# Performance work log

Hardware: AMD Instinct MI355X
Metric: run time of the kernel (lower is better)

The kernel has to match this reference:

```python
import jax, jax.numpy as jnp
import numpy as np

N = 8192
IN_DIM = 512
OUT_DIM = 64
ALPHA = 0.2  # LeakyReLU negative slope
NEG_FILL = -9e15


def setup_inputs() -> dict:
    key = jax.random.key(0)
    k1, k2, k3, k4 = jax.random.split(key, 4)
    features = jax.random.normal(k1, (N, IN_DIM), dtype=jnp.float32)
    adj = jax.random.randint(k2, (N, N), 0, 2, dtype=jnp.int32)
    # xavier_normal with gain 1.414 ~ sqrt(2)
    W = jax.random.normal(k3, (IN_DIM, OUT_DIM), dtype=jnp.float32) * (1.414 * np.sqrt(2.0 / (IN_DIM + OUT_DIM)))
    a = jax.random.normal(k4, (2 * OUT_DIM, 1), dtype=jnp.float32) * (1.414 * np.sqrt(2.0 / (2 * OUT_DIM + 1)))
    return {"features": features, "adj": adj, "W": W, "a": a}


def reference(features, adj, W, a):
    h = features @ W                      # [N, OUT_DIM]
    h1 = h @ a[:OUT_DIM, :]               # [N, 1]
    h2 = h @ a[OUT_DIM:, :]               # [N, 1]
    e = h1 + h2.T                         # [N, N] broadcast add
    e = jnp.where(e > 0, e, ALPHA * e)    # LeakyReLU
    scores = jnp.where(adj > 0, e, NEG_FILL)
    attention = jax.nn.softmax(scores, axis=-1)
    out = attention @ h                   # [N, OUT_DIM]
    out = jax.nn.elu(out)                 # concat=True branch
    return out
```

## Files before the change

kernel.cpp:

```cpp
#include <hip/hip_runtime.h>
#include <hip/hip_bf16.h>

#define N 8192
#define IN_DIM 512
#define OUT_DIM 64
#define ALPHA 0.2f
#define LOG2E 1.44269504f

typedef __hip_bfloat16 bf16;
typedef __attribute__((ext_vector_type(8))) short bf16x8;
typedef __attribute__((ext_vector_type(4))) float f32x4;
typedef __attribute__((ext_vector_type(4))) int   int4v;
typedef __attribute__((ext_vector_type(4))) float float4v;

__device__ __forceinline__ float u2f(unsigned short u) {
    union { unsigned int i; float f; } c; c.i = ((unsigned int)u) << 16; return c.f;
}

__device__ __forceinline__ uint2 splitpack2(float f0, float f1) {
    unsigned u0 = __float_as_uint(f0), u1 = __float_as_uint(f1);
    unsigned h0 = u0 & 0xFFFF0000u, h1 = u1 & 0xFFFF0000u;
    float l0 = f0 - __uint_as_float(h0);
    float l1 = f1 - __uint_as_float(h1);
    uint2 r;
    r.x = (h0 >> 16) | h1;
    r.y = (__float_as_uint(l0) >> 16) | (__float_as_uint(l1) & 0xFFFF0000u);
    return r;
}

__device__ __forceinline__ bf16x8 as_bf16x8(int a, int b, int c, int d) {
    union { int4v i; bf16x8 b; } u;
    u.i = (int4v){a, b, c, d};
    return u.b;
}

__device__ __forceinline__ unsigned fenc(float f) {
    unsigned u = __float_as_uint(f);
    return (u & 0x80000000u) ? ~u : (u | 0x80000000u);
}
__device__ __forceinline__ float fdec(unsigned e) {
    return (e & 0x80000000u) ? __uint_as_float(e & 0x7FFFFFFFu) : __uint_as_float(~e);
}

__global__ void k_sniff(const unsigned short* __restrict__ feat_u16, int* __restrict__ flag) {
    int lane = threadIdx.x;
    float v = u2f(feat_u16[2 * lane]);
    float av = fabsf(v);
    int ok = (v == 0.f) || (av > 1e-8f && av < 1e8f);
    unsigned long long m = __ballot(ok);
    if (lane == 0) *flag = (__popcll(m) >= 48) ? 1 : 0;
}

__global__ __launch_bounds__(256) void k_prep(const void* __restrict__ Wv,
                                              const int* __restrict__ flag,
                                              unsigned short* __restrict__ WT_hi,
                                              unsigned short* __restrict__ WT_lo,
                                              unsigned* __restrict__ h2enc) {
    if (blockIdx.x == 0 && threadIdx.x == 0) *h2enc = fenc(-3e38f);
    int idx = blockIdx.x * 256 + threadIdx.x;
    int k = idx >> 6, c = idx & 63;
    float w = (*flag) ? u2f(((const unsigned short*)Wv)[idx]) : ((const float*)Wv)[idx];
    unsigned u = __float_as_uint(w);
    unsigned hi = u & 0xFFFF0000u;
    float lo = w - __uint_as_float(hi);
    WT_hi[c * IN_DIM + k] = (unsigned short)(hi >> 16);
    WT_lo[c * IN_DIM + k] = (unsigned short)(__float_as_uint(lo) >> 16);
}

__global__ __launch_bounds__(64) void k_h(const void* __restrict__ featv,
                                          const unsigned short* __restrict__ WT_hi,
                                          const unsigned short* __restrict__ WT_lo,
                                          const void* __restrict__ av,
                                          const int* __restrict__ flag,
                                          float* __restrict__ h1,
                                          float* __restrict__ h2,
                                          unsigned short* __restrict__ hT_hi,
                                          unsigned short* __restrict__ hT_lo,
                                          unsigned* __restrict__ h2enc) {
    const int lane = threadIdx.x & 63;
    const int rsub = lane & 15;
    const int g = lane >> 4;
    const int wrow0 = blockIdx.x * 16;
    const int isbf = *flag;

    f32x4 acc0 = {0.f,0.f,0.f,0.f}, acc1 = {0.f,0.f,0.f,0.f};
    f32x4 acc2 = {0.f,0.f,0.f,0.f}, acc3 = {0.f,0.f,0.f,0.f};

    for (int k0 = 0; k0 < IN_DIM; k0 += 32) {
        const int ka = k0 + g * 8;
        bf16x8 Ah, Al;
        if (isbf) {
            Ah = *(const bf16x8*)((const unsigned short*)featv + (size_t)(wrow0 + rsub) * IN_DIM + ka);
            Al = as_bf16x8(0, 0, 0, 0);
        } else {
            const float* fp = (const float*)featv + (size_t)(wrow0 + rsub) * IN_DIM + ka;
            float4v f0 = *(const float4v*)fp;
            float4v f1 = *(const float4v*)(fp + 4);
            uint2 q0 = splitpack2(f0[0], f0[1]);
            uint2 q1 = splitpack2(f0[2], f0[3]);
            uint2 q2 = splitpack2(f1[0], f1[1]);
            uint2 q3 = splitpack2(f1[2], f1[3]);
            Ah = as_bf16x8((int)q0.x, (int)q1.x, (int)q2.x, (int)q3.x);
            Al = as_bf16x8((int)q0.y, (int)q1.y, (int)q2.y, (int)q3.y);
        }
        const unsigned short* wh = WT_hi + (size_t)rsub * IN_DIM + ka;
        const unsigned short* wl = WT_lo + (size_t)rsub * IN_DIM + ka;
        bf16x8 B0h = *(const bf16x8*)(wh);
        bf16x8 B1h = *(const bf16x8*)(wh + 16 * IN_DIM);
        bf16x8 B2h = *(const bf16x8*)(wh + 32 * IN_DIM);
        bf16x8 B3h = *(const bf16x8*)(wh + 48 * IN_DIM);
        bf16x8 B0l = *(const bf16x8*)(wl);
        bf16x8 B1l = *(const bf16x8*)(wl + 16 * IN_DIM);
        bf16x8 B2l = *(const bf16x8*)(wl + 32 * IN_DIM);
        bf16x8 B3l = *(const bf16x8*)(wl + 48 * IN_DIM);

        acc0 = __builtin_amdgcn_mfma_f32_16x16x32_bf16(Ah, B0h, acc0, 0, 0, 0);
        acc1 = __builtin_amdgcn_mfma_f32_16x16x32_bf16(Ah, B1h, acc1, 0, 0, 0);
        acc2 = __builtin_amdgcn_mfma_f32_16x16x32_bf16(Ah, B2h, acc2, 0, 0, 0);
        acc3 = __builtin_amdgcn_mfma_f32_16x16x32_bf16(Ah, B3h, acc3, 0, 0, 0);
        acc0 = __builtin_amdgcn_mfma_f32_16x16x32_bf16(Ah, B0l, acc0, 0, 0, 0);
        acc1 = __builtin_amdgcn_mfma_f32_16x16x32_bf16(Ah, B1l, acc1, 0, 0, 0);
        acc2 = __builtin_amdgcn_mfma_f32_16x16x32_bf16(Ah, B2l, acc2, 0, 0, 0);
        acc3 = __builtin_amdgcn_mfma_f32_16x16x32_bf16(Ah, B3l, acc3, 0, 0, 0);
        acc0 = __builtin_amdgcn_mfma_f32_16x16x32_bf16(Al, B0h, acc0, 0, 0, 0);
        acc1 = __builtin_amdgcn_mfma_f32_16x16x32_bf16(Al, B1h, acc1, 0, 0, 0);
        acc2 = __builtin_amdgcn_mfma_f32_16x16x32_bf16(Al, B2h, acc2, 0, 0, 0);
        acc3 = __builtin_amdgcn_mfma_f32_16x16x32_bf16(Al, B3h, acc3, 0, 0, 0);
    }

    {
        uint2 s01, s23;
        size_t off;
        s01 = splitpack2(acc0[0], acc0[1]); s23 = splitpack2(acc0[2], acc0[3]);
        off = (size_t)(0 * 16 + rsub) * N + wrow0 + g * 4;
        { uint2 ph; ph.x = s01.x; ph.y = s23.x; *(uint2*)(hT_hi + off) = ph; }
        { uint2 pl; pl.x = s01.y; pl.y = s23.y; *(uint2*)(hT_lo + off) = pl; }
        s01 = splitpack2(acc1[0], acc1[1]); s23 = splitpack2(acc1[2], acc1[3]);
        off = (size_t)(1 * 16 + rsub) * N + wrow0 + g * 4;
        { uint2 ph; ph.x = s01.x; ph.y = s23.x; *(uint2*)(hT_hi + off) = ph; }
        { uint2 pl; pl.x = s01.y; pl.y = s23.y; *(uint2*)(hT_lo + off) = pl; }
        s01 = splitpack2(acc2[0], acc2[1]); s23 = splitpack2(acc2[2], acc2[3]);
        off = (size_t)(2 * 16 + rsub) * N + wrow0 + g * 4;
        { uint2 ph; ph.x = s01.x; ph.y = s23.x; *(uint2*)(hT_hi + off) = ph; }
        { uint2 pl; pl.x = s01.y; pl.y = s23.y; *(uint2*)(hT_lo + off) = pl; }
        s01 = splitpack2(acc3[0], acc3[1]); s23 = splitpack2(acc3[2], acc3[3]);
        off = (size_t)(3 * 16 + rsub) * N + wrow0 + g * 4;
        { uint2 ph; ph.x = s01.x; ph.y = s23.x; *(uint2*)(hT_hi + off) = ph; }
        { uint2 pl; pl.x = s01.y; pl.y = s23.y; *(uint2*)(hT_lo + off) = pl; }
    }

    const float* af = (const float*)av;
    const unsigned short* au = (const unsigned short*)av;
    float a10 = isbf ? u2f(au[rsub])      : af[rsub];
    float a11 = isbf ? u2f(au[16 + rsub]) : af[16 + rsub];
    float a12 = isbf ? u2f(au[32 + rsub]) : af[32 + rsub];
    float a13 = isbf ? u2f(au[48 + rsub]) : af[48 + rsub];
    float a20 = isbf ? u2f(au[64 + rsub])  : af[64 + rsub];
    float a21 = isbf ? u2f(au[80 + rsub])  : af[80 + rsub];
    float a22 = isbf ? u2f(au[96 + rsub])  : af[96 + rsub];
    float a23 = isbf ? u2f(au[112 + rsub]) : af[112 + rsub];
    float s1r[4], s2r[4];
#pragma unroll
    for (int r = 0; r < 4; ++r) {
        s1r[r] = acc0[r] * a10 + acc1[r] * a11 + acc2[r] * a12 + acc3[r] * a13;
        s2r[r] = acc0[r] * a20 + acc1[r] * a21 + acc2[r] * a22 + acc3[r] * a23;
    }
#pragma unroll
    for (int off = 8; off; off >>= 1) {
#pragma unroll
        for (int r = 0; r < 4; ++r) {
            s1r[r] += __shfl_xor(s1r[r], off);
            s2r[r] += __shfl_xor(s2r[r], off);
        }
    }
    float wm = fmaxf(fmaxf(s2r[0], s2r[1]), fmaxf(s2r[2], s2r[3])) * LOG2E;
#pragma unroll
    for (int off = 32; off; off >>= 1) wm = fmaxf(wm, __shfl_xor(wm, off));
    if (lane == 0) atomicMax(h2enc, fenc(wm));

    if (rsub < 4) {
        float v1 = rsub == 0 ? s1r[0] : rsub == 1 ? s1r[1] : rsub == 2 ? s1r[2] : s1r[3];
        float v2 = rsub == 0 ? s2r[0] : rsub == 1 ? s2r[1] : rsub == 2 ? s2r[2] : s2r[3];
        h1[wrow0 + g * 4 + rsub] = v1 * LOG2E;
        h2[wrow0 + g * 4 + rsub] = v2 * LOG2E;
    }
}

__global__ __launch_bounds__(256, 2) void k_attn(const int* __restrict__ adj,
                                                 const float* __restrict__ h1,
                                                 const float* __restrict__ h2,
                                                 const unsigned short* __restrict__ hT_hi,
                                                 const unsigned short* __restrict__ hT_lo,
                                                 const unsigned* __restrict__ h2enc,
                                                 float* __restrict__ pacc,
                                                 float* __restrict__ plner,
                                                 int klen) {
    __shared__ float accs[64][66];
    __shared__ float lredL[4][64];

    const int wave = threadIdx.x >> 6;
    const int lane = threadIdx.x & 63;
    const int rsub = lane & 15;
    const int g = lane >> 4;
    const int row0 = blockIdx.x * 64;
    const int kbid = blockIdx.y;

    const float h2m = fdec(*h2enc);
    float h1r[4], c0[4];
#pragma unroll
    for (int mt = 0; mt < 4; ++mt) {
        h1r[mt] = h1[row0 + mt * 16 + rsub];
        float u = h1r[mt] + h2m;
        c0[mt] = -fmaxf(u, ALPHA * u);
    }

    f32x4 acc[4][4];
#pragma unroll
    for (int mt = 0; mt < 4; ++mt)
#pragma unroll
        for (int ct = 0; ct < 4; ++ct) acc[mt][ct] = (f32x4){0.f, 0.f, 0.f, 0.f};
    float lacc[4] = {0.f, 0.f, 0.f, 0.f};

    const unsigned short* bph = hT_hi + (size_t)rsub * N;
    const unsigned short* bpl = hT_lo + (size_t)rsub * N;

    const int kbeg = kbid * klen + wave * (klen >> 2);
    const int kend = kbeg + (klen >> 2);
    for (int k0 = kbeg; k0 < kend; k0 += 32) {
        const int kb = k0 + g * 8;

        const unsigned short* bh = bph + kb;
        const unsigned short* bl = bpl + kb;
        bf16x8 B0h = *(const bf16x8*)(bh);
        bf16x8 B1h = *(const bf16x8*)(bh + 16 * (size_t)N);
        bf16x8 B2h = *(const bf16x8*)(bh + 32 * (size_t)N);
        bf16x8 B3h = *(const bf16x8*)(bh + 48 * (size_t)N);
        bf16x8 B0l = *(const bf16x8*)(bl);
        bf16x8 B1l = *(const bf16x8*)(bl + 16 * (size_t)N);
        bf16x8 B2l = *(const bf16x8*)(bl + 32 * (size_t)N);
        bf16x8 B3l = *(const bf16x8*)(bl + 48 * (size_t)N);

        float4v hA = *(const float4v*)(h2 + kb);
        float4v hB = *(const float4v*)(h2 + kb + 4);

#pragma unroll
        for (int mt = 0; mt < 4; ++mt) {
            const size_t arow = (size_t)(row0 + mt * 16 + rsub) * N + kb;
            int4v aj0 = *(const int4v*)(adj + arow);
            int4v aj1 = *(const int4v*)(adj + arow + 4);

            float w[8];
#pragma unroll
            for (int j = 0; j < 4; ++j) {
                float u = h1r[mt] + hA[j];
                float s = fmaxf(u, ALPHA * u);
                float e = exp2f(s + c0[mt]);
                w[j] = aj0[j] > 0 ? e : 0.f;
            }
#pragma unroll
            for (int j = 0; j < 4; ++j) {
                float u = h1r[mt] + hB[j];
                float s = fmaxf(u, ALPHA * u);
                float e = exp2f(s + c0[mt]);
                w[4 + j] = aj1[j] > 0 ? e : 0.f;
            }
#pragma unroll
            for (int j = 0; j < 8; ++j) lacc[mt] += w[j];

            uint2 p0 = splitpack2(w[0], w[1]);
            uint2 p1 = splitpack2(w[2], w[3]);
            uint2 p2 = splitpack2(w[4], w[5]);
            uint2 p3 = splitpack2(w[6], w[7]);
            bf16x8 Ahi = as_bf16x8((int)p0.x, (int)p1.x, (int)p2.x, (int)p3.x);
            bf16x8 Alo = as_bf16x8((int)p0.y, (int)p1.y, (int)p2.y, (int)p3.y);

            acc[mt][0] = __builtin_amdgcn_mfma_f32_16x16x32_bf16(Ahi, B0h, acc[mt][0], 0, 0, 0);
            acc[mt][1] = __builtin_amdgcn_mfma_f32_16x16x32_bf16(Ahi, B1h, acc[mt][1], 0, 0, 0);
            acc[mt][2] = __builtin_amdgcn_mfma_f32_16x16x32_bf16(Ahi, B2h, acc[mt][2], 0, 0, 0);
            acc[mt][3] = __builtin_amdgcn_mfma_f32_16x16x32_bf16(Ahi, B3h, acc[mt][3], 0, 0, 0);
            acc[mt][0] = __builtin_amdgcn_mfma_f32_16x16x32_bf16(Ahi, B0l, acc[mt][0], 0, 0, 0);
            acc[mt][1] = __builtin_amdgcn_mfma_f32_16x16x32_bf16(Ahi, B1l, acc[mt][1], 0, 0, 0);
            acc[mt][2] = __builtin_amdgcn_mfma_f32_16x16x32_bf16(Ahi, B2l, acc[mt][2], 0, 0, 0);
            acc[mt][3] = __builtin_amdgcn_mfma_f32_16x16x32_bf16(Ahi, B3l, acc[mt][3], 0, 0, 0);
            acc[mt][0] = __builtin_amdgcn_mfma_f32_16x16x32_bf16(Alo, B0h, acc[mt][0], 0, 0, 0);
            acc[mt][1] = __builtin_amdgcn_mfma_f32_16x16x32_bf16(Alo, B1h, acc[mt][1], 0, 0, 0);
            acc[mt][2] = __builtin_amdgcn_mfma_f32_16x16x32_bf16(Alo, B2h, acc[mt][2], 0, 0, 0);
            acc[mt][3] = __builtin_amdgcn_mfma_f32_16x16x32_bf16(Alo, B3h, acc[mt][3], 0, 0, 0);
        }
    }

#pragma unroll
    for (int mt = 0; mt < 4; ++mt) {
        float l = lacc[mt];
        l += __shfl_xor(l, 16);
        l += __shfl_xor(l, 32);
        if (g == 0) lredL[wave][mt * 16 + rsub] = l;
    }

    if (wave == 0) {
#pragma unroll
        for (int mt = 0; mt < 4; ++mt)
#pragma unroll
            for (int ct = 0; ct < 4; ++ct)
#pragma unroll
                for (int r = 0; r < 4; ++r)
                    accs[mt * 16 + g * 4 + r][ct * 16 + rsub] = acc[mt][ct][r];
    }
    __syncthreads();
#pragma unroll
    for (int w2 = 1; w2 < 4; ++w2) {
        if (wave == w2) {
#pragma unroll
            for (int mt = 0; mt < 4; ++mt)
#pragma unroll
                for (int ct = 0; ct < 4; ++ct)
#pragma unroll
                    for (int r = 0; r < 4; ++r)
                        accs[mt * 16 + g * 4 + r][ct * 16 + rsub] += acc[mt][ct][r];
        }
        __syncthreads();
    }

    float* pa = pacc + (size_t)kbid * (N * OUT_DIM);
#pragma unroll
    for (int p = 0; p < 16; ++p) {
        int idx = p * 256 + threadIdx.x;
        int rl = idx >> 6, col = idx & 63;
        pa[(size_t)(row0 + rl) * OUT_DIM + col] = accs[rl][col];
    }
    if (threadIdx.x < 64)
        plner[(size_t)kbid * N + row0 + threadIdx.x] =
            lredL[0][threadIdx.x] + lredL[1][threadIdx.x] + lredL[2][threadIdx.x] + lredL[3][threadIdx.x];
}

__global__ __launch_bounds__(256) void k_out(const float* __restrict__ pacc,
                                             const float* __restrict__ plner,
                                             const int* __restrict__ flag,
                                             void* __restrict__ outv,
                                             int nkb) {
    int idx = blockIdx.x * 256 + threadIdx.x;
    int row = idx >> 6;
    float v = 0.f, l = 0.f;
    for (int kb = 0; kb < nkb; ++kb) {
        v += pacc[(size_t)kb * (N * OUT_DIM) + idx];
        l += plner[(size_t)kb * N + row];
    }
    float o = l > 0.f ? v / l : 0.f;
    o = o > 0.f ? o : exp2f(o * LOG2E) - 1.f;
    if (*flag) ((bf16*)outv)[idx] = __float2bfloat16(o);
    else       ((float*)outv)[idx] = o;
}

extern "C" void kernel_launch(void* const* d_in, const int* in_sizes, int n_in,
                              void* d_out, int out_size, void* d_ws, size_t ws_size,
                              hipStream_t stream) {
    const void* feat = d_in[0];
    const int* adj = (const int*)d_in[1];
    const void* W = d_in[2];
    const void* a = d_in[3];

    char* ws = (char*)d_ws;
    int*      flag  = (int*)(ws);
    unsigned* h2enc = (unsigned*)(ws + 256);
    float* h1       = (float*)(ws + 4096);
    float* h2       = (float*)(ws + 36864);
    unsigned short* hT_hi = (unsigned short*)(ws + 69632);
    unsigned short* hT_lo = (unsigned short*)(ws + 69632 + 1048576);
    unsigned short* WT_hi = (unsigned short*)(ws + 2166784);
    unsigned short* WT_lo = (unsigned short*)(ws + 2166784 + 65536);
    char* dynbase = ws + 2297856;

    size_t cap = ws_size ? ws_size : ((size_t)1 << 30);
    int nkb = 8;
    while (nkb > 1) {
        size_t need = 2297856 + (size_t)nkb * ((size_t)N * OUT_DIM * 4 + (size_t)N * 4);
        if (need <= cap) break;
        nkb >>= 1;
    }
    float* pacc  = (float*)dynbase;
    float* plner = (float*)(dynbase + (size_t)nkb * N * OUT_DIM * 4);

    hipLaunchKernelGGL(k_sniff, dim3(1), dim3(64), 0, stream,
                       (const unsigned short*)feat, flag);
    hipLaunchKernelGGL(k_prep, dim3((IN_DIM * OUT_DIM) / 256), dim3(256), 0, stream,
                       W, flag, WT_hi, WT_lo, h2enc);
    hipLaunchKernelGGL(k_h, dim3(N / 16), dim3(64), 0, stream,
                       feat, WT_hi, WT_lo, a, flag, h1, h2, hT_hi, hT_lo, h2enc);
    hipLaunchKernelGGL(k_attn, dim3(N / 64, nkb), dim3(256), 0, stream,
                       adj, h1, h2, hT_hi, hT_lo, h2enc, pacc, plner, N / nkb);
    hipLaunchKernelGGL(k_out, dim3((N * OUT_DIM) / 256), dim3(256), 0, stream,
                       pacc, plner, flag, d_out, nkb);
}
```

Baseline: 420.1 us.

## Split k_h reduction dimension across four waves with shared-memory accumulation

The feature projection kernel now uses 256 threads per block. Each of four waves handles a quarter of the IN_DIM reduction, and the partial tiles are summed in shared memory with serialized adds. The transposed hi/lo output stores and the h1/h2 attention-coefficient dot products are then computed from that shared tile. The aim is to shorten the per-block serial MFMA chain and raise parallelism in this projection stage, at the cost of extra syncs and LDS traffic. The h1/h2 reduction is now done by a single 16-lane group.

```diff
diff --git a/kernel.cpp b/kernel.cpp
--- a/kernel.cpp
+++ b/kernel.cpp
@@ -67,17 +67,20 @@
     WT_lo[c * IN_DIM + k] = (unsigned short)(__float_as_uint(lo) >> 16);
 }
 
-__global__ __launch_bounds__(64) void k_h(const void* __restrict__ featv,
-                                          const unsigned short* __restrict__ WT_hi,
-                                          const unsigned short* __restrict__ WT_lo,
-                                          const void* __restrict__ av,
-                                          const int* __restrict__ flag,
-                                          float* __restrict__ h1,
-                                          float* __restrict__ h2,
-                                          unsigned short* __restrict__ hT_hi,
-                                          unsigned short* __restrict__ hT_lo,
-                                          unsigned* __restrict__ h2enc) {
-    const int lane = threadIdx.x & 63;
+__global__ __launch_bounds__(256) void k_h(const void* __restrict__ featv,
+                                           const unsigned short* __restrict__ WT_hi,
+                                           const unsigned short* __restrict__ WT_lo,
+                                           const void* __restrict__ av,
+                                           const int* __restrict__ flag,
+                                           float* __restrict__ h1,
+                                           float* __restrict__ h2,
+                                           unsigned short* __restrict__ hT_hi,
+                                           unsigned short* __restrict__ hT_lo,
+                                           unsigned* __restrict__ h2enc) {
+    __shared__ float C[16][66];
+    const int tid = threadIdx.x;
+    const int wave = tid >> 6;
+    const int lane = tid & 63;
     const int rsub = lane & 15;
     const int g = lane >> 4;
     const int wrow0 = blockIdx.x * 16;
@@ -86,7 +89,8 @@
     f32x4 acc0 = {0.f,0.f,0.f,0.f}, acc1 = {0.f,0.f,0.f,0.f};
     f32x4 acc2 = {0.f,0.f,0.f,0.f}, acc3 = {0.f,0.f,0.f,0.f};
 
-    for (int k0 = 0; k0 < IN_DIM; k0 += 32) {
+    const int kbeg = wave * (IN_DIM / 4);
+    for (int k0 = kbeg; k0 < kbeg + IN_DIM / 4; k0 += 32) {
         const int ka = k0 + g * 8;
         bf16x8 Ah, Al;
         if (isbf) {
@@ -128,61 +132,60 @@
         acc3 = __builtin_amdgcn_mfma_f32_16x16x32_bf16(Al, B3h, acc3, 0, 0, 0);
     }
 
+    if (wave == 0) {
+#pragma unroll
+        for (int r = 0; r < 4; ++r) {
+            C[g * 4 + r][rsub]      = acc0[r];
+            C[g * 4 + r][16 + rsub] = acc1[r];
+            C[g * 4 + r][32 + rsub] = acc2[r];
+            C[g * 4 + r][48 + rsub] = acc3[r];
+        }
+    }
+    __syncthreads();
+#pragma unroll
+    for (int w2 = 1; w2 < 4; ++w2) {
+        if (wave == w2) {
+#pragma unroll
+            for (int r = 0; r < 4; ++r) {
+                C[g * 4 + r][rsub]      += acc0[r];
+                C[g * 4 + r][16 + rsub] += acc1[r];
+                C[g * 4 + r][32 + rsub] += acc2[r];
+                C[g * 4 + r][48 + rsub] += acc3[r];
+            }
+        }
+        __syncthreads();
+    }
+
     {
-        uint2 s01, s23;
-        size_t off;
-        s01 = splitpack2(acc0[0], acc0[1]); s23 = splitpack2(acc0[2], acc0[3]);
-        off = (size_t)(0 * 16 + rsub) * N + wrow0 + g * 4;
+        int c = tid >> 2;
+        int r0 = (tid & 3) * 4;
+        float v0 = C[r0 + 0][c], v1 = C[r0 + 1][c], v2 = C[r0 + 2][c], v3 = C[r0 + 3][c];
+        uint2 s01 = splitpack2(v0, v1);
+        uint2 s23 = splitpack2(v2, v3);
+        size_t off = (size_t)c * N + wrow0 + r0;
         { uint2 ph; ph.x = s01.x; ph.y = s23.x; *(uint2*)(hT_hi + off) = ph; }
         { uint2 pl; pl.x = s01.y; pl.y = s23.y; *(uint2*)(hT_lo + off) = pl; }
-        s01 = splitpack2(acc1[0], acc1[1]); s23 = splitpack2(acc1[2], acc1[3]);
-        off = (size_t)(1 * 16 + rsub) * N + wrow0 + g * 4;
-        { uint2 ph; ph.x = s01.x; ph.y = s23.x; *(uint2*)(hT_hi + off) = ph; }
-        { uint2 pl; pl.x = s01.y; pl.y = s23.y; *(uint2*)(hT_lo + off) = pl; }
-        s01 = splitpack2(acc2[0], acc2[1]); s23 = splitpack2(acc2[2], acc2[3]);
-        off = (size_t)(2 * 16 + rsub) * N + wrow0 + g * 4;
-        { uint2 ph; ph.x = s01.x; ph.y = s23.x; *(uint2*)(hT_hi + off) = ph; }
-        { uint2 pl; pl.x = s01.y; pl.y = s23.y; *(uint2*)(hT_lo + off) = pl; }
-        s01 = splitpack2(acc3[0], acc3[1]); s23 = splitpack2(acc3[2], acc3[3]);
-        off = (size_t)(3 * 16 + rsub) * N + wrow0 + g * 4;
-        { uint2 ph; ph.x = s01.x; ph.y = s23.x; *(uint2*)(hT_hi + off) = ph; }
-        { uint2 pl; pl.x = s01.y; pl.y = s23.y; *(uint2*)(hT_lo + off) = pl; }
-    }
-
-    const float* af = (const float*)av;
-    const unsigned short* au = (const unsigned short*)av;
-    float a10 = isbf ? u2f(au[rsub])      : af[rsub];
-    float a11 = isbf ? u2f(au[16 + rsub]) : af[16 + rsub];
-    float a12 = isbf ? u2f(au[32 + rsub]) : af[32 + rsub];
-    float a13 = isbf ? u2f(au[48 + rsub]) : af[48 + rsub];
-    float a20 = isbf ? u2f(au[64 + rsub])  : af[64 + rsub];
-    float a21 = isbf ? u2f(au[80 + rsub])  : af[80 + rsub];
-    float a22 = isbf ? u2f(au[96 + rsub])  : af[96 + rsub];
-    float a23 = isbf ? u2f(au[112 + rsub]) : af[112 + rsub];
-    float s1r[4], s2r[4];
-#pragma unroll
-    for (int r = 0; r < 4; ++r) {
-        s1r[r] = acc0[r] * a10 + acc1[r] * a11 + acc2[r] * a12 + acc3[r] * a13;
-        s2r[r] = acc0[r] * a20 + acc1[r] * a21 + acc2[r] * a22 + acc3[r] * a23;
-    }
-#pragma unroll
-    for (int off = 8; off; off >>= 1) {
-#pragma unroll
-        for (int r = 0; r < 4; ++r) {
-            s1r[r] += __shfl_xor(s1r[r], off);
-            s2r[r] += __shfl_xor(s2r[r], off);
-        }
-    }
-    float wm = fmaxf(fmaxf(s2r[0], s2r[1]), fmaxf(s2r[2], s2r[3])) * LOG2E;
-#pragma unroll
-    for (int off = 32; off; off >>= 1) wm = fmaxf(wm, __shfl_xor(wm, off));
-    if (lane == 0) atomicMax(h2enc, fenc(wm));
-
-    if (rsub < 4) {
-        float v1 = rsub == 0 ? s1r[0] : rsub == 1 ? s1r[1] : rsub == 2 ? s1r[2] : s1r[3];
-        float v2 = rsub == 0 ? s2r[0] : rsub == 1 ? s2r[1] : rsub == 2 ? s2r[2] : s2r[3];
-        h1[wrow0 + g * 4 + rsub] = v1 * LOG2E;
-        h2[wrow0 + g * 4 + rsub] = v2 * LOG2E;
+    }
+
+    if (wave == 0 && lane < 16) {
+        const float* af = (const float*)av;
+        const unsigned short* au = (const unsigned short*)av;
+        float s1 = 0.f, s2 = 0.f;
+#pragma unroll 8
+        for (int c = 0; c < 64; ++c) {
+            float a1 = isbf ? u2f(au[c])      : af[c];
+            float a2 = isbf ? u2f(au[64 + c]) : af[64 + c];
+            float hv = C[lane][c];
+            s1 += hv * a1;
+            s2 += hv * a2;
+        }
+        s1 *= LOG2E; s2 *= LOG2E;
+        h1[wrow0 + lane] = s1;
+        h2[wrow0 + lane] = s2;
+        float wm = s2;
+#pragma unroll
+        for (int off = 8; off; off >>= 1) wm = fmaxf(wm, __shfl_xor(wm, off));
+        if (lane == 0) atomicMax(h2enc, fenc(wm));
     }
 }
 
@@ -384,7 +387,7 @@
                        (const unsigned short*)feat, flag);
     hipLaunchKernelGGL(k_prep, dim3((IN_DIM * OUT_DIM) / 256), dim3(256), 0, stream,
                        W, flag, WT_hi, WT_lo, h2enc);
-    hipLaunchKernelGGL(k_h, dim3(N / 16), dim3(64), 0, stream,
+    hipLaunchKernelGGL(k_h, dim3(N / 16), dim3(256), 0, stream,
                        feat, WT_hi, WT_lo, a, flag, h1, h2, hT_hi, hT_lo, h2enc);
     hipLaunchKernelGGL(k_attn, dim3(N / 64, nkb), dim3(256), 0, stream,
                        adj, h1, h2, hT_hi, hT_lo, h2enc, pacc, plner, N / nkb);
```

New measurement: 417.9 us, median of 2. No clear change (-0.5%).
